# Kernel tuning notes

Measured on AMD Instinct MI355X. Metric: run time of the kernel, lower is better.

Reference implementation:

```python
import jax, jax.numpy as jnp
import numpy as np

DIM = 2048
ATT_DIM = 2048
N_HEADS = 16
HEAD_DIM = ATT_DIM // N_HEADS  # 128


def setup_inputs() -> dict:
    key = jax.random.key(0)
    k1, k2, k3 = jax.random.split(key, 3)
    tgt_len = 2048
    x = jax.random.normal(k1, (tgt_len, DIM), dtype=jnp.float32)
    # nn.Linear weights: [out_features, in_features], no bias
    w_in = jax.random.normal(k2, (3 * ATT_DIM, DIM), dtype=jnp.float32) * (1.0 / np.sqrt(DIM))
    w_out = jax.random.normal(k3, (DIM, ATT_DIM), dtype=jnp.float32) * (1.0 / np.sqrt(ATT_DIM))
    return {"x": x, "w_in": w_in, "w_out": w_out, "tgt_len": tgt_len}


def reference(x, w_in, w_out, tgt_len):
    # qkv projection: Linear -> x @ W^T, then split into thirds
    qkv = x @ w_in.T                      # [T, 3*att_dim]
    q, k, v = jnp.split(qkv, 3, axis=-1)  # each [T, att_dim]
    # [T, H, Dh] -> [H, T, Dh]
    q = q.reshape(tgt_len, N_HEADS, HEAD_DIM).transpose(1, 0, 2)
    k = k.reshape(tgt_len, N_HEADS, HEAD_DIM).transpose(1, 0, 2)
    v = v.reshape(tgt_len, N_HEADS, HEAD_DIM).transpose(1, 0, 2)
    scaling = 1.0 / jnp.sqrt(jnp.asarray(HEAD_DIM, dtype=x.dtype))
    scores = jnp.einsum("htd,hsd->hts", q, k) * scaling  # [H, T, T]
    attn = jax.nn.softmax(scores, axis=-1)
    ctx = jnp.einsum("hts,hsd->htd", attn, v)             # [H, T, Dh]
    ctx = ctx.transpose(1, 0, 2).reshape(tgt_len, ATT_DIM)
    return ctx @ w_out.T                                   # [T, dim]
```

## Files before the change

### kernel.cpp

```cpp
#include <hip/hip_runtime.h>

#define T_LEN 2048
#define DIM 2048
#define NH 16
#define HD 128
#define QKV_LD 6144

typedef __attribute__((ext_vector_type(8))) short short8;
typedef __attribute__((ext_vector_type(4))) float f32x4;
typedef __attribute__((ext_vector_type(4))) float float4v;
typedef __attribute__((ext_vector_type(4))) unsigned short ushort4v;
typedef __attribute__((ext_vector_type(2))) unsigned int uint2v;

static __device__ __forceinline__ unsigned short f2bf(float f) {
  unsigned u = __builtin_bit_cast(unsigned, f);
  u += 0x7fffu + ((u >> 16) & 1u);
  return (unsigned short)(u >> 16);
}

static __device__ __forceinline__ float bf2f(unsigned short u) {
  unsigned x = ((unsigned)u) << 16;
  return __builtin_bit_cast(float, x);
}

static __device__ __forceinline__ float max3f(float a, float b, float c) {
  return fmaxf(fmaxf(a, b), c);
}

static __device__ __forceinline__ f32x4 mfma16(short8 a, short8 b, f32x4 c) {
  return __builtin_amdgcn_mfma_f32_16x16x32_bf16(a, b, c, 0, 0, 0);
}

#define GLDS16(SRC, DST)                                                            \
  __builtin_amdgcn_global_load_lds((__attribute__((address_space(1))) void*)(SRC),  \
                                   (__attribute__((address_space(3))) void*)(DST),  \
                                   16, 0, 0)

__global__ void cast_f32_bf16(const float* __restrict__ in,
                              unsigned short* __restrict__ out, int n4) {
  int i = blockIdx.x * blockDim.x + threadIdx.x;
  const int stride = gridDim.x * blockDim.x;
  for (; i < n4; i += stride) {
    float4v f = ((const float4v*)in)[i];
    ushort4v o;
    o.x = f2bf(f.x); o.y = f2bf(f.y); o.z = f2bf(f.z); o.w = f2bf(f.w);
    ((ushort4v*)out)[i] = o;
  }
}

template <int OUT_BF16>
__global__ __launch_bounds__(256) void gemm_bt_128(
    const unsigned short* __restrict__ A,
    const unsigned short* __restrict__ B,
    void* __restrict__ Cv, int M, int N, int K) {
  __shared__ unsigned short As[128 * 64];
  __shared__ unsigned short Bs[128 * 64];
  const int tid = threadIdx.x;
  const int wave = tid >> 6;
  const int lane = tid & 63;
  const int l15 = lane & 15, l16 = lane >> 4;
  const int bm = blockIdx.y * 128;
  const int bn = blockIdx.x * 128;
  const int wr = wave >> 1, wc = wave & 1;

  f32x4 acc[4][4] = {};

  int srow[4], scol[4];
#pragma unroll
  for (int i = 0; i < 4; ++i) {
    int lin = i * 4096 + tid * 16;
    int row = lin >> 7;
    int cb = lin & 127;
    srow[i] = row;
    scol[i] = (cb ^ ((row & 7) << 4)) >> 1;
  }

  for (int k0 = 0; k0 < K; k0 += 64) {
#pragma unroll
    for (int i = 0; i < 4; ++i) {
      GLDS16(A + (size_t)(bm + srow[i]) * K + k0 + scol[i], As + i * 2048 + wave * 512);
      GLDS16(B + (size_t)(bn + srow[i]) * K + k0 + scol[i], Bs + i * 2048 + wave * 512);
    }
    __syncthreads();
#pragma unroll
    for (int kk = 0; kk < 2; ++kk) {
      const int cb = kk * 64 + l16 * 16;
      short8 af[4], bfr[4];
#pragma unroll
      for (int m = 0; m < 4; ++m) {
        int row = wr * 64 + m * 16 + l15;
        af[m] = *(const short8*)((const char*)As + row * 128 + (cb ^ ((row & 7) << 4)));
      }
#pragma unroll
      for (int n = 0; n < 4; ++n) {
        int row = wc * 64 + n * 16 + l15;
        bfr[n] = *(const short8*)((const char*)Bs + row * 128 + (cb ^ ((row & 7) << 4)));
      }
#pragma unroll
      for (int m = 0; m < 4; ++m)
#pragma unroll
        for (int n = 0; n < 4; ++n)
          acc[m][n] = mfma16(af[m], bfr[n], acc[m][n]);
    }
    __syncthreads();
  }

#pragma unroll
  for (int m = 0; m < 4; ++m)
#pragma unroll
    for (int n = 0; n < 4; ++n) {
      int row = bm + wr * 64 + m * 16 + l16 * 4;
      int col = bn + wc * 64 + n * 16 + l15;
#pragma unroll
      for (int j = 0; j < 4; ++j) {
        if (OUT_BF16)
          ((unsigned short*)Cv)[(size_t)(row + j) * N + col] = f2bf(acc[m][n][j]);
        else
          ((float*)Cv)[(size_t)(row + j) * N + col] = acc[m][n][j];
      }
    }
}

__global__ __launch_bounds__(256) void transpose_v(
    const unsigned short* __restrict__ qkv, unsigned short* __restrict__ vt) {
  __shared__ unsigned short t[64 * 128];
  const int tid = threadIdx.x;
  const int h = blockIdx.y;
  const int s0 = blockIdx.x * 64;
#pragma unroll
  for (int i = 0; i < 4; ++i) {
    int lin = i * 2048 + tid * 8;
    int row = lin >> 7, col = lin & 127;
    char* dst = (char*)t + row * 256 + ((col * 2) ^ (((row >> 3) & 7) << 4));
    *(short8*)dst =
        *(const short8*)(qkv + (size_t)(s0 + row) * QKV_LD + 2 * DIM + h * HD + col);
  }
  __syncthreads();
#pragma unroll
  for (int i2 = 0; i2 < 4; ++i2) {
    int d = (tid >> 3) + i2 * 32;
    int sb = (tid & 7) * 8;
    short8 v;
#pragma unroll
    for (int j = 0; j < 8; ++j) {
      int s = sb + j;
      v[j] = *(const short*)((const char*)t + s * 256 + ((d * 2) ^ (((s >> 3) & 7) << 4)));
    }
    *(short8*)(vt + ((size_t)h * HD + d) * T_LEN + s0 + sb) = v;
  }
}

__global__ __launch_bounds__(256) void attn_fwd(
    const unsigned short* __restrict__ qkv,
    const unsigned short* __restrict__ vt,
    unsigned short* __restrict__ po,
    float* __restrict__ ml) {
  __shared__ unsigned short Ks[64 * 128];
  __shared__ unsigned short Vs[128 * 64];
  __shared__ unsigned short Ps[4 * 16 * 64];
  const int tid = threadIdx.x;
  const int wave = tid >> 6;
  const int lane = tid & 63;
  const int l15 = lane & 15, l16 = lane >> 4;

  const int wg = blockIdx.y * 64 + blockIdx.x;
  const int swz = (wg & 7) * 128 + (wg >> 3);
  const int h = swz >> 6;
  const int half = (swz >> 5) & 1;
  const int q0 = (swz & 31) * 64 + wave * 16;
  const int s_begin = half * (T_LEN / 2);
  const float SCL = 0.08838834764831845f * 1.4426950408889634f;

  short8 qf[4];
#pragma unroll
  for (int kk = 0; kk < 4; ++kk)
    qf[kk] = *(const short8*)(qkv + (size_t)(q0 + l15) * QKV_LD + h * HD + kk * 32 + l16 * 8);

  f32x4 acc_o[8] = {};
  float m_r = -1e30f;
  float l_r = 0.f;

  const unsigned short* kp[4];
  const unsigned short* vp[4];
#pragma unroll
  for (int i = 0; i < 4; ++i) {
    int lin = i * 4096 + tid * 16;
    int r = lin >> 8;
    int cb = lin & 255;
    kp[i] = qkv + 2048 + h * HD + (size_t)(s_begin + r) * QKV_LD + ((cb ^ ((r & 7) << 4)) >> 1);
    r = lin >> 7;
    cb = lin & 127;
    vp[i] = vt + (size_t)h * HD * T_LEN + (size_t)r * T_LEN + s_begin +
            ((cb ^ ((r & 7) << 4)) >> 1);
  }

  const int NT = (T_LEN / 2) / 64;
  for (int t = 0; t < NT; ++t) {
#pragma unroll
    for (int i = 0; i < 4; ++i) {
      GLDS16(kp[i], Ks + i * 2048 + wave * 512);
      GLDS16(vp[i], Vs + i * 2048 + wave * 512);
      kp[i] += 64 * QKV_LD;
      vp[i] += 64;
    }
    __syncthreads();

    f32x4 st[4] = {};
    __builtin_amdgcn_s_setprio(1);
#pragma unroll
    for (int c = 0; c < 4; ++c) {
#pragma unroll
      for (int kk = 0; kk < 4; ++kk) {
        int row = c * 16 + l15;
        int cb = kk * 64 + l16 * 16;
        short8 kf = *(const short8*)((const char*)Ks + row * 256 + (cb ^ ((row & 7) << 4)));
        st[c] = mfma16(kf, qf[kk], st[c]);
      }
    }
    __builtin_amdgcn_s_setprio(0);

    float ma = max3f(st[0][0], st[0][1], st[0][2]);
    float mb = max3f(st[0][3], st[1][0], st[1][1]);
    float mc = max3f(st[1][2], st[1][3], st[2][0]);
    float md = max3f(st[2][1], st[2][2], st[2][3]);
    float me = max3f(st[3][0], st[3][1], st[3][2]);
    float pmax = fmaxf(max3f(ma, mb, mc), max3f(md, me, st[3][3]));
    pmax *= SCL;
    pmax = fmaxf(pmax, __shfl_xor(pmax, 16));
    pmax = fmaxf(pmax, __shfl_xor(pmax, 32));

    if (!__all(pmax - m_r <= 8.0f)) {
      float nm = fmaxf(m_r, pmax);
      float corr = __builtin_amdgcn_exp2f(m_r - nm);
      m_r = nm;
      l_r *= corr;
      float cj[4];
#pragma unroll
      for (int j = 0; j < 4; ++j) cj[j] = __shfl(corr, l16 * 4 + j);
#pragma unroll
      for (int d = 0; d < 8; ++d)
#pragma unroll
        for (int j = 0; j < 4; ++j) acc_o[d][j] *= cj[j];
    }

    float p[4][4];
#pragma unroll
    for (int c = 0; c < 4; ++c)
#pragma unroll
      for (int j = 0; j < 4; ++j)
        p[c][j] = __builtin_amdgcn_exp2f(st[c][j] * SCL - m_r);
    float s01 = (p[0][0] + p[0][1]) + (p[0][2] + p[0][3]);
    float s23 = (p[1][0] + p[1][1]) + (p[1][2] + p[1][3]);
    float s45 = (p[2][0] + p[2][1]) + (p[2][2] + p[2][3]);
    float s67 = (p[3][0] + p[3][1]) + (p[3][2] + p[3][3]);
    float tsum = (s01 + s23) + (s45 + s67);
    tsum += __shfl_xor(tsum, 16);
    tsum += __shfl_xor(tsum, 32);
    l_r += tsum;

    char* pbase = (char*)Ps + wave * 2048;
#pragma unroll
    for (int c = 0; c < 4; ++c) {
      uint2v w;
      w.x = (unsigned)f2bf(p[c][0]) | ((unsigned)f2bf(p[c][1]) << 16);
      w.y = (unsigned)f2bf(p[c][2]) | ((unsigned)f2bf(p[c][3]) << 16);
      int off = l15 * 128 + c * 32 + l16 * 8;
      *(uint2v*)(pbase + (off ^ ((l15 & 7) << 4))) = w;
    }

    __builtin_amdgcn_s_setprio(1);
#pragma unroll
    for (int kk = 0; kk < 2; ++kk) {
      int cb = kk * 64 + l16 * 16;
      short8 pa = *(const short8*)(pbase + l15 * 128 + (cb ^ ((l15 & 7) << 4)));
#pragma unroll
      for (int d = 0; d < 8; ++d) {
        int row = d * 16 + l15;
        short8 vb = *(const short8*)((const char*)Vs + row * 128 + (cb ^ ((row & 7) << 4)));
        acc_o[d] = mfma16(pa, vb, acc_o[d]);
      }
    }
    __builtin_amdgcn_s_setprio(0);

    __syncthreads();
  }

  const size_t pbaseo = ((size_t)half * NH * T_LEN + (size_t)h * T_LEN) * HD;
#pragma unroll
  for (int d = 0; d < 8; ++d)
#pragma unroll
    for (int j = 0; j < 4; ++j) {
      int q = q0 + l16 * 4 + j;
      po[pbaseo + (size_t)q * HD + d * 16 + l15] = f2bf(acc_o[d][j]);
    }
  if (l16 == 0) {
    size_t mlbase = ((size_t)half * NH * T_LEN + (size_t)h * T_LEN + q0 + l15) * 2;
    ml[mlbase] = m_r;
    ml[mlbase + 1] = l_r;
  }
}

__global__ __launch_bounds__(256) void attn_combine(
    const unsigned short* __restrict__ po, const float* __restrict__ ml,
    unsigned short* __restrict__ ctx) {
  const int g = blockIdx.x * 256 + threadIdx.x;
  const int hq = g >> 4;
  const int oct = g & 15;
  const float m0 = ml[hq * 2], l0 = ml[hq * 2 + 1];
  const float m1 = ml[NH * T_LEN * 2 + hq * 2], l1 = ml[NH * T_LEN * 2 + hq * 2 + 1];
  const float m = fmaxf(m0, m1);
  float a0 = __builtin_amdgcn_exp2f(m0 - m);
  float a1 = __builtin_amdgcn_exp2f(m1 - m);
  const float rl = 1.0f / (l0 * a0 + l1 * a1);
  a0 *= rl; a1 *= rl;
  const short8 o0 = *(const short8*)(po + (size_t)hq * HD + oct * 8);
  const short8 o1 = *(const short8*)(po + (size_t)NH * T_LEN * HD + (size_t)hq * HD + oct * 8);
  short8 w;
#pragma unroll
  for (int j = 0; j < 8; ++j)
    w[j] = (short)f2bf(bf2f((unsigned short)o0[j]) * a0 + bf2f((unsigned short)o1[j]) * a1);
  const int h = hq >> 11, q = hq & (T_LEN - 1);
  *(short8*)(ctx + (size_t)q * DIM + h * HD + oct * 8) = w;
}

extern "C" void kernel_launch(void* const* d_in, const int* in_sizes, int n_in,
                              void* d_out, int out_size, void* d_ws, size_t ws_size,
                              hipStream_t stream) {
  const float* x = (const float*)d_in[0];
  const float* w_in = (const float*)d_in[1];
  const float* w_out = (const float*)d_in[2];

  char* ws = (char*)d_ws;
  unsigned short* xbf  = (unsigned short*)(ws + 0);
  unsigned short* wibf = (unsigned short*)(ws + 8388608);
  unsigned short* wobf = (unsigned short*)(ws + 33554432);
  unsigned short* qkv  = (unsigned short*)(ws + 41943040);
  unsigned short* ctx  = (unsigned short*)(ws + 67108864);
  unsigned short* vt   = (unsigned short*)(ws + 75497472);
  unsigned short* po   = (unsigned short*)(ws + 0);
  float*          ml   = (float*)(ws + 16777216);

  cast_f32_bf16<<<2048, 256, 0, stream>>>(x, xbf, (T_LEN * DIM) / 4);
  cast_f32_bf16<<<2048, 256, 0, stream>>>(w_in, wibf, (3 * DIM * DIM) / 4);
  cast_f32_bf16<<<2048, 256, 0, stream>>>(w_out, wobf, (DIM * DIM) / 4);

  gemm_bt_128<1><<<dim3(48, 16), 256, 0, stream>>>(xbf, wibf, (void*)qkv, T_LEN, 3 * DIM, DIM);
  transpose_v<<<dim3(32, 16), 256, 0, stream>>>(qkv, vt);
  attn_fwd<<<dim3(64, 16), 256, 0, stream>>>(qkv, vt, po, ml);
  attn_combine<<<2048, 256, 0, stream>>>(po, ml, ctx);
  gemm_bt_128<0><<<dim3(16, 16), 256, 0, stream>>>(ctx, wobf, d_out, T_LEN, DIM, DIM);
}
```

Before: 204.1 us.

## Process two query tiles per wave and double-buffer K/V loads in attention

Each wave now handles 32 query rows instead of 16, so every K and V fragment read from shared memory feeds two MFMAs, and the grid is halved to 512 workgroups. K tiles are double-buffered through async global-to-LDS loads, while V is prefetched into registers and written to LDS after the compute step. The goal is to cut LDS traffic per FLOP and hide global load latency. The cost is higher register pressure, more LDS use, an extra barrier per iteration, and fewer workgroups to fill the GPU.

```diff
diff --git a/kernel.cpp b/kernel.cpp
--- a/kernel.cpp
+++ b/kernel.cpp
@@ -155,57 +155,85 @@
     const unsigned short* __restrict__ vt,
     unsigned short* __restrict__ po,
     float* __restrict__ ml) {
-  __shared__ unsigned short Ks[64 * 128];
+  __shared__ unsigned short Ks[2][64 * 128];
   __shared__ unsigned short Vs[128 * 64];
-  __shared__ unsigned short Ps[4 * 16 * 64];
+  __shared__ unsigned short Ps[4 * 32 * 64];
   const int tid = threadIdx.x;
   const int wave = tid >> 6;
   const int lane = tid & 63;
   const int l15 = lane & 15, l16 = lane >> 4;
 
-  const int wg = blockIdx.y * 64 + blockIdx.x;
-  const int swz = (wg & 7) * 128 + (wg >> 3);
-  const int h = swz >> 6;
-  const int half = (swz >> 5) & 1;
-  const int q0 = (swz & 31) * 64 + wave * 16;
-  const int s_begin = half * (T_LEN / 2);
+  const int wg = blockIdx.y * 32 + blockIdx.x;
+  const int swz = (wg & 7) * 64 + (wg >> 3);
+  const int h = swz >> 5;
+  const int khalf = (swz >> 4) & 1;
+  const int q0 = (swz & 15) * 128 + wave * 32;
+  const int s_begin = khalf * (T_LEN / 2);
   const float SCL = 0.08838834764831845f * 1.4426950408889634f;
 
-  short8 qf[4];
-#pragma unroll
-  for (int kk = 0; kk < 4; ++kk)
-    qf[kk] = *(const short8*)(qkv + (size_t)(q0 + l15) * QKV_LD + h * HD + kk * 32 + l16 * 8);
-
-  f32x4 acc_o[8] = {};
-  float m_r = -1e30f;
-  float l_r = 0.f;
+  short8 qf[2][4];
+#pragma unroll
+  for (int qh = 0; qh < 2; ++qh)
+#pragma unroll
+    for (int kk = 0; kk < 4; ++kk)
+      qf[qh][kk] = *(const short8*)(qkv + (size_t)(q0 + qh * 16 + l15) * QKV_LD +
+                                    h * HD + kk * 32 + l16 * 8);
+
+  f32x4 acc0[8] = {}, acc1[8] = {};
+  float m_r0 = -1e30f, m_r1 = -1e30f;
+  float l_r0 = 0.f, l_r1 = 0.f;
 
   const unsigned short* kp[4];
-  const unsigned short* vp[4];
 #pragma unroll
   for (int i = 0; i < 4; ++i) {
     int lin = i * 4096 + tid * 16;
     int r = lin >> 8;
     int cb = lin & 255;
-    kp[i] = qkv + 2048 + h * HD + (size_t)(s_begin + r) * QKV_LD + ((cb ^ ((r & 7) << 4)) >> 1);
-    r = lin >> 7;
-    cb = lin & 127;
-    vp[i] = vt + (size_t)h * HD * T_LEN + (size_t)r * T_LEN + s_begin +
+    kp[i] = qkv + 2048 + h * HD + (size_t)(s_begin + r) * QKV_LD +
             ((cb ^ ((r & 7) << 4)) >> 1);
   }
+  const unsigned short* vp[4];
+  int woff[4];
+#pragma unroll
+  for (int i = 0; i < 4; ++i) {
+    int d = wave * 32 + i * 8 + (lane >> 3);
+    vp[i] = vt + (size_t)h * HD * T_LEN + (size_t)d * T_LEN + s_begin + (lane & 7) * 8;
+    woff[i] = d * 128 + (((lane & 7) * 16) ^ ((d & 7) << 4));
+  }
+
+  short8 vreg[4];
+#pragma unroll
+  for (int i = 0; i < 4; ++i) {
+    vreg[i] = *(const short8*)vp[i];
+    vp[i] += 64;
+  }
+#pragma unroll
+  for (int i = 0; i < 4; ++i) {
+    GLDS16(kp[i], Ks[0] + i * 2048 + wave * 512);
+    kp[i] += 64 * QKV_LD;
+  }
+#pragma unroll
+  for (int i = 0; i < 4; ++i) *(short8*)((char*)Vs + woff[i]) = vreg[i];
+  __syncthreads();
 
   const int NT = (T_LEN / 2) / 64;
+  int cur = 0;
   for (int t = 0; t < NT; ++t) {
-#pragma unroll
-    for (int i = 0; i < 4; ++i) {
-      GLDS16(kp[i], Ks + i * 2048 + wave * 512);
-      GLDS16(vp[i], Vs + i * 2048 + wave * 512);
-      kp[i] += 64 * QKV_LD;
-      vp[i] += 64;
-    }
-    __syncthreads();
-
-    f32x4 st[4] = {};
+    if (t + 1 < NT) {
+#pragma unroll
+      for (int i = 0; i < 4; ++i) {
+        GLDS16(kp[i], Ks[cur ^ 1] + i * 2048 + wave * 512);
+        kp[i] += 64 * QKV_LD;
+      }
+#pragma unroll
+      for (int i = 0; i < 4; ++i) {
+        vreg[i] = *(const short8*)vp[i];
+        vp[i] += 64;
+      }
+    }
+    const unsigned short* ks = Ks[cur];
+
+    f32x4 st0[4] = {}, st1[4] = {};
     __builtin_amdgcn_s_setprio(1);
 #pragma unroll
     for (int c = 0; c < 4; ++c) {
@@ -213,90 +241,130 @@
       for (int kk = 0; kk < 4; ++kk) {
         int row = c * 16 + l15;
         int cb = kk * 64 + l16 * 16;
-        short8 kf = *(const short8*)((const char*)Ks + row * 256 + (cb ^ ((row & 7) << 4)));
-        st[c] = mfma16(kf, qf[kk], st[c]);
+        short8 kf = *(const short8*)((const char*)ks + row * 256 + (cb ^ ((row & 7) << 4)));
+        st0[c] = mfma16(kf, qf[0][kk], st0[c]);
+        st1[c] = mfma16(kf, qf[1][kk], st1[c]);
       }
     }
     __builtin_amdgcn_s_setprio(0);
 
-    float ma = max3f(st[0][0], st[0][1], st[0][2]);
-    float mb = max3f(st[0][3], st[1][0], st[1][1]);
-    float mc = max3f(st[1][2], st[1][3], st[2][0]);
-    float md = max3f(st[2][1], st[2][2], st[2][3]);
-    float me = max3f(st[3][0], st[3][1], st[3][2]);
-    float pmax = fmaxf(max3f(ma, mb, mc), max3f(md, me, st[3][3]));
-    pmax *= SCL;
-    pmax = fmaxf(pmax, __shfl_xor(pmax, 16));
-    pmax = fmaxf(pmax, __shfl_xor(pmax, 32));
-
-    if (!__all(pmax - m_r <= 8.0f)) {
-      float nm = fmaxf(m_r, pmax);
-      float corr = __builtin_amdgcn_exp2f(m_r - nm);
-      m_r = nm;
-      l_r *= corr;
-      float cj[4];
-#pragma unroll
-      for (int j = 0; j < 4; ++j) cj[j] = __shfl(corr, l16 * 4 + j);
+    float ma0 = max3f(st0[0][0], st0[0][1], st0[0][2]);
+    float mb0 = max3f(st0[0][3], st0[1][0], st0[1][1]);
+    float mc0 = max3f(st0[1][2], st0[1][3], st0[2][0]);
+    float md0 = max3f(st0[2][1], st0[2][2], st0[2][3]);
+    float me0 = max3f(st0[3][0], st0[3][1], st0[3][2]);
+    float pmax0 = fmaxf(max3f(ma0, mb0, mc0), max3f(md0, me0, st0[3][3])) * SCL;
+    float ma1 = max3f(st1[0][0], st1[0][1], st1[0][2]);
+    float mb1 = max3f(st1[0][3], st1[1][0], st1[1][1]);
+    float mc1 = max3f(st1[1][2], st1[1][3], st1[2][0]);
+    float md1 = max3f(st1[2][1], st1[2][2], st1[2][3]);
+    float me1 = max3f(st1[3][0], st1[3][1], st1[3][2]);
+    float pmax1 = fmaxf(max3f(ma1, mb1, mc1), max3f(md1, me1, st1[3][3])) * SCL;
+    pmax0 = fmaxf(pmax0, __shfl_xor(pmax0, 16));
+    pmax0 = fmaxf(pmax0, __shfl_xor(pmax0, 32));
+    pmax1 = fmaxf(pmax1, __shfl_xor(pmax1, 16));
+    pmax1 = fmaxf(pmax1, __shfl_xor(pmax1, 32));
+
+    float need = fmaxf(pmax0 - m_r0, pmax1 - m_r1);
+    if (!__all(need <= 8.0f)) {
+      float nm0 = fmaxf(m_r0, pmax0);
+      float corr0 = __builtin_amdgcn_exp2f(m_r0 - nm0);
+      m_r0 = nm0; l_r0 *= corr0;
+      float nm1 = fmaxf(m_r1, pmax1);
+      float corr1 = __builtin_amdgcn_exp2f(m_r1 - nm1);
+      m_r1 = nm1; l_r1 *= corr1;
+      float cj0[4], cj1[4];
+#pragma unroll
+      for (int j = 0; j < 4; ++j) {
+        cj0[j] = __shfl(corr0, l16 * 4 + j);
+        cj1[j] = __shfl(corr1, l16 * 4 + j);
+      }
 #pragma unroll
       for (int d = 0; d < 8; ++d)
 #pragma unroll
-        for (int j = 0; j < 4; ++j) acc_o[d][j] *= cj[j];
-    }
-
-    float p[4][4];
+        for (int j = 0; j < 4; ++j) {
+          acc0[d][j] *= cj0[j];
+          acc1[d][j] *= cj1[j];
+        }
+    }
+
+    float p0[4][4], p1[4][4];
 #pragma unroll
     for (int c = 0; c < 4; ++c)
 #pragma unroll
-      for (int j = 0; j < 4; ++j)
-        p[c][j] = __builtin_amdgcn_exp2f(st[c][j] * SCL - m_r);
-    float s01 = (p[0][0] + p[0][1]) + (p[0][2] + p[0][3]);
-    float s23 = (p[1][0] + p[1][1]) + (p[1][2] + p[1][3]);
-    float s45 = (p[2][0] + p[2][1]) + (p[2][2] + p[2][3]);
-    float s67 = (p[3][0] + p[3][1]) + (p[3][2] + p[3][3]);
-    float tsum = (s01 + s23) + (s45 + s67);
-    tsum += __shfl_xor(tsum, 16);
-    tsum += __shfl_xor(tsum, 32);
-    l_r += tsum;
-
-    char* pbase = (char*)Ps + wave * 2048;
+      for (int j = 0; j < 4; ++j) {
+        p0[c][j] = __builtin_amdgcn_exp2f(st0[c][j] * SCL - m_r0);
+        p1[c][j] = __builtin_amdgcn_exp2f(st1[c][j] * SCL - m_r1);
+      }
+    float ts0 = ((p0[0][0] + p0[0][1]) + (p0[0][2] + p0[0][3])) +
+                ((p0[1][0] + p0[1][1]) + (p0[1][2] + p0[1][3])) +
+                (((p0[2][0] + p0[2][1]) + (p0[2][2] + p0[2][3])) +
+                 ((p0[3][0] + p0[3][1]) + (p0[3][2] + p0[3][3])));
+    float ts1 = ((p1[0][0] + p1[0][1]) + (p1[0][2] + p1[0][3])) +
+                ((p1[1][0] + p1[1][1]) + (p1[1][2] + p1[1][3])) +
+                (((p1[2][0] + p1[2][1]) + (p1[2][2] + p1[2][3])) +
+                 ((p1[3][0] + p1[3][1]) + (p1[3][2] + p1[3][3])));
+    ts0 += __shfl_xor(ts0, 16);
+    ts0 += __shfl_xor(ts0, 32);
+    ts1 += __shfl_xor(ts1, 16);
+    ts1 += __shfl_xor(ts1, 32);
+    l_r0 += ts0;
+    l_r1 += ts1;
+
+    char* pbase = (char*)Ps + wave * 4096;
 #pragma unroll
     for (int c = 0; c < 4; ++c) {
-      uint2v w;
-      w.x = (unsigned)f2bf(p[c][0]) | ((unsigned)f2bf(p[c][1]) << 16);
-      w.y = (unsigned)f2bf(p[c][2]) | ((unsigned)f2bf(p[c][3]) << 16);
-      int off = l15 * 128 + c * 32 + l16 * 8;
-      *(uint2v*)(pbase + (off ^ ((l15 & 7) << 4))) = w;
+      uint2v w0, w1;
+      w0.x = (unsigned)f2bf(p0[c][0]) | ((unsigned)f2bf(p0[c][1]) << 16);
+      w0.y = (unsigned)f2bf(p0[c][2]) | ((unsigned)f2bf(p0[c][3]) << 16);
+      w1.x = (unsigned)f2bf(p1[c][0]) | ((unsigned)f2bf(p1[c][1]) << 16);
+      w1.y = (unsigned)f2bf(p1[c][2]) | ((unsigned)f2bf(p1[c][3]) << 16);
+      int off0 = l15 * 128 + c * 32 + l16 * 8;
+      int off1 = (16 + l15) * 128 + c * 32 + l16 * 8;
+      *(uint2v*)(pbase + (off0 ^ ((l15 & 7) << 4))) = w0;
+      *(uint2v*)(pbase + (off1 ^ ((l15 & 7) << 4))) = w1;
     }
 
     __builtin_amdgcn_s_setprio(1);
 #pragma unroll
     for (int kk = 0; kk < 2; ++kk) {
       int cb = kk * 64 + l16 * 16;
-      short8 pa = *(const short8*)(pbase + l15 * 128 + (cb ^ ((l15 & 7) << 4)));
+      short8 pa0 = *(const short8*)(pbase + ((l15 * 128 + cb) ^ ((l15 & 7) << 4)));
+      short8 pa1 = *(const short8*)(pbase + (((16 + l15) * 128 + cb) ^ ((l15 & 7) << 4)));
 #pragma unroll
       for (int d = 0; d < 8; ++d) {
         int row = d * 16 + l15;
         short8 vb = *(const short8*)((const char*)Vs + row * 128 + (cb ^ ((row & 7) << 4)));
-        acc_o[d] = mfma16(pa, vb, acc_o[d]);
+        acc0[d] = mfma16(pa0, vb, acc0[d]);
+        acc1[d] = mfma16(pa1, vb, acc1[d]);
       }
     }
     __builtin_amdgcn_s_setprio(0);
 
     __syncthreads();
-  }
-
-  const size_t pbaseo = ((size_t)half * NH * T_LEN + (size_t)h * T_LEN) * HD;
+    if (t + 1 < NT) {
+#pragma unroll
+      for (int i = 0; i < 4; ++i) *(short8*)((char*)Vs + woff[i]) = vreg[i];
+    }
+    __syncthreads();
+    cur ^= 1;
+  }
+
+  const size_t pb = ((size_t)khalf * NH * T_LEN + (size_t)h * T_LEN) * HD;
 #pragma unroll
   for (int d = 0; d < 8; ++d)
 #pragma unroll
     for (int j = 0; j < 4; ++j) {
-      int q = q0 + l16 * 4 + j;
-      po[pbaseo + (size_t)q * HD + d * 16 + l15] = f2bf(acc_o[d][j]);
+      int qa = q0 + l16 * 4 + j;
+      int qb = q0 + 16 + l16 * 4 + j;
+      po[pb + (size_t)qa * HD + d * 16 + l15] = f2bf(acc0[d][j]);
+      po[pb + (size_t)qb * HD + d * 16 + l15] = f2bf(acc1[d][j]);
     }
   if (l16 == 0) {
-    size_t mlbase = ((size_t)half * NH * T_LEN + (size_t)h * T_LEN + q0 + l15) * 2;
-    ml[mlbase] = m_r;
-    ml[mlbase + 1] = l_r;
+    size_t b0 = ((size_t)khalf * NH * T_LEN + (size_t)h * T_LEN + q0 + l15) * 2;
+    size_t b1 = ((size_t)khalf * NH * T_LEN + (size_t)h * T_LEN + q0 + 16 + l15) * 2;
+    ml[b0] = m_r0; ml[b0 + 1] = l_r0;
+    ml[b1] = m_r1; ml[b1 + 1] = l_r1;
   }
 }
 
@@ -346,7 +414,7 @@
 
   gemm_bt_128<1><<<dim3(48, 16), 256, 0, stream>>>(xbf, wibf, (void*)qkv, T_LEN, 3 * DIM, DIM);
   transpose_v<<<dim3(32, 16), 256, 0, stream>>>(qkv, vt);
-  attn_fwd<<<dim3(64, 16), 256, 0, stream>>>(qkv, vt, po, ml);
+  attn_fwd<<<dim3(32, 16), 256, 0, stream>>>(qkv, vt, po, ml);
   attn_combine<<<2048, 256, 0, stream>>>(po, ml, ctx);
   gemm_bt_128<0><<<dim3(16, 16), 256, 0, stream>>>(ctx, wobf, d_out, T_LEN, DIM, DIM);
 }
```

New measurement: 214.0 us. 1.05x slower.
